# Performance work log

Hardware: AMD Instinct MI355X
Metric: run time of the kernel (lower is better)

The kernel has to match this reference:

```python
import jax, jax.numpy as jnp
import numpy as np

ROWS = 256
COLS = 256
EPS = 1e-8


def _radius_bins(rows, cols):
    # Same construction as SpectralLoss.__init__: integer radius per rfft bin,
    # ifftshifted along the row axis to match torch.rfft layout.
    shift_rows = rows // 2
    cols_onesided = cols // 2 + 1
    idx = np.indices((rows, cols_onesided)) - np.array([[[shift_rows]], [[0]]])
    r = np.sqrt(idx[0] ** 2 + idx[1] ** 2).astype(int)
    r = np.fft.ifftshift(r, axes=0)
    return r  # [rows, cols_onesided], values in [0, r_max]


def setup_inputs() -> dict:
    key = jax.random.key(0)
    k1, k2 = jax.random.split(key)
    r = _radius_bins(ROWS, COLS)
    vector_length = int(r.max()) + 1  # 182
    data = jax.random.normal(k1, (128, 3, ROWS, COLS), dtype=jnp.float32)
    mean = jax.random.uniform(k2, (vector_length,), dtype=jnp.float32)
    radius = jnp.asarray(r, dtype=jnp.int32)
    return {"data": data, "mean": mean, "radius": radius}


def reference(data, mean, radius):
    L = mean.shape[0]  # vector_length = r_max + 1
    # RGB -> luma (as in SpectralLoss.fft)
    gray = 0.299 * data[:, 0] + 0.587 * data[:, 1] + 0.114 * data[:, 2]  # [B,H,W]
    f = jnp.fft.rfft2(gray)  # [B, H, W//2+1]
    power = f.real ** 2 + f.imag ** 2  # sum of squared re/im parts
    fft_abs = 20.0 * jnp.log(power + EPS)  # [B, H, Wc]
    # Radial histogram: segment-mean keyed on integer radius (replaces the
    # original dense one-hot mask broadcast of shape [B, L, H, Wc]).
    seg = radius.reshape(-1)  # [N] with N = H*Wc
    B = fft_abs.shape[0]
    flat = fft_abs.reshape(B, -1).T  # [N, B]
    sums = jax.ops.segment_sum(flat, seg, num_segments=L)  # [L, B]
    counts = jax.ops.segment_sum(jnp.ones_like(flat[:, :1]), seg, num_segments=L)  # [L, 1]
    profile = (sums / counts).T  # [B, L]
    # Per-sample min-max normalization (same order of ops as torch code)
    profile = profile - jnp.min(profile, axis=1, keepdims=True)
    profile = profile / jnp.max(profile, axis=1, keepdims=True)
    # L1 loss with reduction='sum' against the target mean profile
    return jnp.sum(jnp.abs(profile - mean[None, :]))
```

## Files before the change

### kernel.cpp

```cpp
#include <hip/hip_runtime.h>
#include <cmath>

#define B_   128
#define H_   256
#define W_   256
#define WC_  129
#define L_   182
#define NG_  17
#define PI_F 3.14159265358979f

__device__ __forceinline__ void fft256x2_wave(float vr[8], float vi[8], int l) {
  float c0, s0;
  __sincosf(-2.f * PI_F * (float)l / 256.f, &s0, &c0);
  float c1 = s0, s1 = -c0;
  float c2 = c0 * c0 - s0 * s0, s2 = 2.f * c0 * s0;
  #pragma unroll
  for (int f = 0; f < 8; f += 4) {
    float ur = vr[f+0] + vr[f+2], ui = vi[f+0] + vi[f+2];
    float dr = vr[f+0] - vr[f+2], di = vi[f+0] - vi[f+2];
    vr[f+0] = ur; vi[f+0] = ui;
    vr[f+2] = dr * c0 - di * s0; vi[f+2] = dr * s0 + di * c0;
    ur = vr[f+1] + vr[f+3]; ui = vi[f+1] + vi[f+3];
    dr = vr[f+1] - vr[f+3]; di = vi[f+1] - vi[f+3];
    vr[f+1] = ur; vi[f+1] = ui;
    vr[f+3] = dr * c1 - di * s1; vi[f+3] = dr * s1 + di * c1;
    ur = vr[f+0] + vr[f+1]; ui = vi[f+0] + vi[f+1];
    dr = vr[f+0] - vr[f+1]; di = vi[f+0] - vi[f+1];
    vr[f+0] = ur; vi[f+0] = ui;
    vr[f+1] = dr * c2 - di * s2; vi[f+1] = dr * s2 + di * c2;
    ur = vr[f+2] + vr[f+3]; ui = vi[f+2] + vi[f+3];
    dr = vr[f+2] - vr[f+3]; di = vi[f+2] - vi[f+3];
    vr[f+2] = ur; vi[f+2] = ui;
    vr[f+3] = dr * c2 - di * s2; vi[f+3] = dr * s2 + di * c2;
  }
  #pragma unroll
  for (int h = 32; h >= 1; h >>= 1) {
    int i = l & (h - 1);
    float c, s;
    __sincosf(-PI_F * (float)i / (float)h, &s, &c);
    bool up = (l & h) != 0;
    float cc = up ? c : 1.f;
    float ss = up ? s : 0.f;
    float sgn = up ? -1.f : 1.f;
    #pragma unroll
    for (int j = 0; j < 8; ++j) {
      float br = __shfl_xor(vr[j], h, 64);
      float bi = __shfl_xor(vi[j], h, 64);
      float tr = fmaf(sgn, vr[j], br);
      float ti = fmaf(sgn, vi[j], bi);
      vr[j] = tr * cc - ti * ss;
      vi[j] = tr * ss + ti * cc;
    }
  }
}

#define P1_PAIRS 8
#define P1_STRIDE 259

__global__ __launch_bounds__(256) void pass1_kernel(
    const float* __restrict__ data, float4* __restrict__ inter4) {
  __shared__ float2 tile[P1_PAIRS * P1_STRIDE];
  int tid = threadIdx.x;
  int w = tid >> 6, l = tid & 63;
  int b = blockIdx.x >> 4;
  int row0 = (blockIdx.x & 15) * 16;
  const float* base = data + (size_t)b * 3 * (H_ * W_);
  float vr[8], vi[8];
  #pragma unroll
  for (int f = 0; f < 2; ++f) {
    int rowA = row0 + 2 * w + 8 * f;
    const float* pR = base + (size_t)rowA * W_;
    #pragma unroll
    for (int j = 0; j < 4; ++j) {
      int i = l + 64 * j;
      float r = pR[i], g = pR[H_ * W_ + i], bl = pR[2 * H_ * W_ + i];
      vr[4 * f + j] = fmaf(0.299f, r, fmaf(0.587f, g, 0.114f * bl));
      r = pR[W_ + i]; g = pR[H_ * W_ + W_ + i]; bl = pR[2 * H_ * W_ + W_ + i];
      vi[4 * f + j] = fmaf(0.299f, r, fmaf(0.587f, g, 0.114f * bl));
    }
  }
  fft256x2_wave(vr, vi, l);
  #pragma unroll
  for (int j = 0; j < 4; ++j) {
    tile[w * P1_STRIDE + l + 64 * j]       = make_float2(vr[j],     vi[j]);
    tile[(w + 4) * P1_STRIDE + l + 64 * j] = make_float2(vr[4 + j], vi[4 + j]);
  }
  __syncthreads();
  for (int f = tid; f < WC_ * P1_PAIRS; f += 256) {
    int k = f >> 3;
    int p = f & 7;
    int qk  = (int)(__brev((unsigned)k) >> 24);
    int qnk = (int)(__brev((unsigned)((256 - k) & 255)) >> 24);
    float2 Zk  = tile[p * P1_STRIDE + qk];
    float2 Znk = tile[p * P1_STRIDE + qnk];
    float4 o;
    o.x = 0.5f * (Zk.x + Znk.x);
    o.y = 0.5f * (Zk.y - Znk.y);
    o.z = 0.5f * (Zk.y + Znk.y);
    o.w = 0.5f * (Znk.x - Zk.x);
    inter4[((((size_t)b * WC_ + k) * H_ + row0) >> 1) + p] = o;
  }
}

__global__ __launch_bounds__(256) void pass2_kernel(
    const float2* __restrict__ inter, const int* __restrict__ radius,
    float* __restrict__ partial, float* __restrict__ cntpart) {
  __shared__ float lbins[L_];
  __shared__ float lcnt[L_];
  int tid = threadIdx.x;
  int wv = tid >> 6, l = tid & 63;
  int b = blockIdx.x / NG_;
  int g = blockIdx.x - b * NG_;
  int k1 = g * 8 + wv;
  int k2 = k1 + 4;
  bool v1 = k1 < WC_, v2 = k2 < WC_;
  bool do_cnt = (b == 0);
  for (int i = tid; i < L_; i += 256) lbins[i] = 0.f;
  if (do_cnt)
    for (int i = tid; i < L_; i += 256) lcnt[i] = 0.f;
  __syncthreads();
  float vr[8], vi[8];
  const float2* p1 = inter + ((size_t)b * WC_ + k1) * H_;
  const float2* p2 = inter + ((size_t)b * WC_ + k2) * H_;
  #pragma unroll
  for (int j = 0; j < 4; ++j) {
    float2 a = v1 ? p1[l + 64 * j] : make_float2(0.f, 0.f);
    float2 c = v2 ? p2[l + 64 * j] : make_float2(0.f, 0.f);
    vr[j] = a.x; vi[j] = a.y;
    vr[4 + j] = c.x; vi[4 + j] = c.y;
  }
  fft256x2_wave(vr, vi, l);
  int rb = 4 * (int)(__brev((unsigned)l) >> 26);
  #pragma unroll
  for (int j = 0; j < 4; ++j) {
    int rf = rb + ((j == 1) ? 2 : (j == 2) ? 1 : j);
    if (v1) {
      int bin = radius[rf * WC_ + k1];
      float pw = vr[j] * vr[j] + vi[j] * vi[j];
      atomicAdd(&lbins[bin], 20.f * __logf(pw + 1e-8f));
      if (do_cnt) atomicAdd(&lcnt[bin], 1.f);
    }
    if (v2) {
      int bin = radius[rf * WC_ + k2];
      float pw = vr[4 + j] * vr[4 + j] + vi[4 + j] * vi[4 + j];
      atomicAdd(&lbins[bin], 20.f * __logf(pw + 1e-8f));
      if (do_cnt) atomicAdd(&lcnt[bin], 1.f);
    }
  }
  __syncthreads();
  float* pp = partial + ((size_t)b * NG_ + g) * L_;
  for (int i = tid; i < L_; i += 256) pp[i] = lbins[i];
  if (do_cnt) {
    float* cp = cntpart + (size_t)g * L_;
    for (int i = tid; i < L_; i += 256) cp[i] = lcnt[i];
  }
}

__global__ __launch_bounds__(64) void loss_kernel(
    const float* __restrict__ partial, const float* __restrict__ cntpart,
    const float* __restrict__ mean, float* __restrict__ lpart) {
  int b = blockIdx.x;
  int l = threadIdx.x;
  const float* pb = partial + (size_t)b * NG_ * L_;
  float s0 = 0.f, s1 = 0.f, s2 = 0.f;
  float n0 = 0.f, n1 = 0.f, n2 = 0.f;
  #pragma unroll 1
  for (int g = 0; g < NG_; ++g) {
    s0 += pb[g * L_ + l];        n0 += cntpart[g * L_ + l];
    s1 += pb[g * L_ + l + 64];   n1 += cntpart[g * L_ + l + 64];
  }
  bool has2 = (l + 128) < L_;
  if (has2) {
    #pragma unroll 1
    for (int g = 0; g < NG_; ++g) {
      s2 += pb[g * L_ + l + 128];
      n2 += cntpart[g * L_ + l + 128];
    }
  }
  float pa = s0 / n0;
  float pc = s1 / n1;
  float pe = has2 ? (s2 / n2) : 0.f;
  float mn = fminf(pa, pc);
  if (has2) mn = fminf(mn, pe);
  #pragma unroll
  for (int h = 32; h >= 1; h >>= 1) mn = fminf(mn, __shfl_xor(mn, h, 64));
  float mxr = fmaxf(pa, pc);
  if (has2) mxr = fmaxf(mxr, pe);
  #pragma unroll
  for (int h = 32; h >= 1; h >>= 1) mxr = fmaxf(mxr, __shfl_xor(mxr, h, 64));
  float mx = mxr - mn;
  float s = fabsf((pa - mn) / mx - mean[l]) +
            fabsf((pc - mn) / mx - mean[l + 64]);
  if (has2) s += fabsf((pe - mn) / mx - mean[l + 128]);
  #pragma unroll
  for (int h = 32; h >= 1; h >>= 1) s += __shfl_xor(s, h, 64);
  if (l == 0) lpart[b] = s;
}

__global__ __launch_bounds__(64) void final_kernel(
    const float* __restrict__ lpart, float* __restrict__ out) {
  int l = threadIdx.x;
  float v = lpart[l] + lpart[l + 64];
  #pragma unroll
  for (int h = 32; h >= 1; h >>= 1) v += __shfl_xor(v, h, 64);
  if (l == 0) out[0] = v;
}

extern "C" void kernel_launch(void* const* d_in, const int* in_sizes, int n_in,
                              void* d_out, int out_size, void* d_ws, size_t ws_size,
                              hipStream_t stream) {
  const float* data   = (const float*)d_in[0];
  const float* mean   = (const float*)d_in[1];
  const int*   radius = (const int*)d_in[2];
  float* out = (float*)d_out;

  float2* inter = (float2*)d_ws;
  size_t inter_bytes = (size_t)B_ * WC_ * H_ * sizeof(float2);
  float* partial = (float*)((char*)d_ws + inter_bytes);
  float* cntpart = partial + (size_t)B_ * NG_ * L_;
  float* lpart   = cntpart + (size_t)NG_ * L_;

  pass1_kernel<<<B_ * 16, 256, 0, stream>>>(data, (float4*)inter);
  pass2_kernel<<<B_ * NG_, 256, 0, stream>>>(inter, radius, partial, cntpart);
  loss_kernel<<<B_, 64, 0, stream>>>(partial, cntpart, mean, lpart);
  final_kernel<<<1, 64, 0, stream>>>(lpart, out);
}
```

Before: 202.4 us.

## Vectorize luma loads through shared memory and fold final reduction into loss kernel

Pass1 now loads the 16-row RGB slab with coalesced float4 reads, computes luma into shared memory, then gathers FFT inputs from LDS instead of scalar strided global reads. The final single-block reduction kernel is removed; the last loss block, detected via an atomic counter reset in pass2, sums the per-sample losses. This cuts one kernel launch and improves global load width at the cost of extra LDS traffic and two barriers.

```diff
diff --git a/kernel.cpp b/kernel.cpp
--- a/kernel.cpp
+++ b/kernel.cpp
@@ -60,25 +60,38 @@
 __global__ __launch_bounds__(256) void pass1_kernel(
     const float* __restrict__ data, float4* __restrict__ inter4) {
   __shared__ float2 tile[P1_PAIRS * P1_STRIDE];
+  float* luma = (float*)tile;
   int tid = threadIdx.x;
   int w = tid >> 6, l = tid & 63;
   int b = blockIdx.x >> 4;
   int row0 = (blockIdx.x & 15) * 16;
-  const float* base = data + (size_t)b * 3 * (H_ * W_);
+  const float* base = data + (size_t)b * 3 * (H_ * W_) + (size_t)row0 * W_;
+  const float4* pr = (const float4*)base;
+  const float4* pg = (const float4*)(base + H_ * W_);
+  const float4* pb = (const float4*)(base + 2 * H_ * W_);
+  #pragma unroll
+  for (int it = 0; it < 4; ++it) {
+    int q = tid + 256 * it;
+    float4 r = pr[q], g = pg[q], bl = pb[q];
+    float4 o;
+    o.x = fmaf(0.299f, r.x, fmaf(0.587f, g.x, 0.114f * bl.x));
+    o.y = fmaf(0.299f, r.y, fmaf(0.587f, g.y, 0.114f * bl.y));
+    o.z = fmaf(0.299f, r.z, fmaf(0.587f, g.z, 0.114f * bl.z));
+    o.w = fmaf(0.299f, r.w, fmaf(0.587f, g.w, 0.114f * bl.w));
+    ((float4*)luma)[q] = o;
+  }
+  __syncthreads();
   float vr[8], vi[8];
   #pragma unroll
   for (int f = 0; f < 2; ++f) {
-    int rowA = row0 + 2 * w + 8 * f;
-    const float* pR = base + (size_t)rowA * W_;
+    int rA = 2 * w + 8 * f;
     #pragma unroll
     for (int j = 0; j < 4; ++j) {
-      int i = l + 64 * j;
-      float r = pR[i], g = pR[H_ * W_ + i], bl = pR[2 * H_ * W_ + i];
-      vr[4 * f + j] = fmaf(0.299f, r, fmaf(0.587f, g, 0.114f * bl));
-      r = pR[W_ + i]; g = pR[H_ * W_ + W_ + i]; bl = pR[2 * H_ * W_ + W_ + i];
-      vi[4 * f + j] = fmaf(0.299f, r, fmaf(0.587f, g, 0.114f * bl));
-    }
-  }
+      vr[4 * f + j] = luma[rA * W_ + l + 64 * j];
+      vi[4 * f + j] = luma[(rA + 1) * W_ + l + 64 * j];
+    }
+  }
+  __syncthreads();
   fft256x2_wave(vr, vi, l);
   #pragma unroll
   for (int j = 0; j < 4; ++j) {
@@ -104,13 +117,15 @@
 
 __global__ __launch_bounds__(256) void pass2_kernel(
     const float2* __restrict__ inter, const int* __restrict__ radius,
-    float* __restrict__ partial, float* __restrict__ cntpart) {
+    float* __restrict__ partial, float* __restrict__ cntpart,
+    unsigned* __restrict__ cnt_sync) {
   __shared__ float lbins[L_];
   __shared__ float lcnt[L_];
   int tid = threadIdx.x;
   int wv = tid >> 6, l = tid & 63;
   int b = blockIdx.x / NG_;
   int g = blockIdx.x - b * NG_;
+  if (blockIdx.x == 0 && tid == 0) cnt_sync[0] = 0u;
   int k1 = g * 8 + wv;
   int k2 = k1 + 4;
   bool v1 = k1 < WC_, v2 = k2 < WC_;
@@ -158,7 +173,8 @@
 
 __global__ __launch_bounds__(64) void loss_kernel(
     const float* __restrict__ partial, const float* __restrict__ cntpart,
-    const float* __restrict__ mean, float* __restrict__ lpart) {
+    const float* __restrict__ mean, float* __restrict__ lpart,
+    unsigned* __restrict__ cnt_sync, float* __restrict__ out) {
   int b = blockIdx.x;
   int l = threadIdx.x;
   const float* pb = partial + (size_t)b * NG_ * L_;
@@ -194,16 +210,24 @@
   if (has2) s += fabsf((pe - mn) / mx - mean[l + 128]);
   #pragma unroll
   for (int h = 32; h >= 1; h >>= 1) s += __shfl_xor(s, h, 64);
-  if (l == 0) lpart[b] = s;
-}
-
-__global__ __launch_bounds__(64) void final_kernel(
-    const float* __restrict__ lpart, float* __restrict__ out) {
-  int l = threadIdx.x;
-  float v = lpart[l] + lpart[l + 64];
-  #pragma unroll
-  for (int h = 32; h >= 1; h >>= 1) v += __shfl_xor(v, h, 64);
-  if (l == 0) out[0] = v;
+  int last = 0;
+  if (l == 0) {
+    lpart[b] = s;
+    __threadfence();
+    unsigned old = __hip_atomic_fetch_add(cnt_sync, 1u, __ATOMIC_ACQ_REL,
+                                          __HIP_MEMORY_SCOPE_AGENT);
+    last = (old == (unsigned)(B_ - 1));
+  }
+  last = __shfl(last, 0, 64);
+  if (last) {
+    float v = __hip_atomic_load(&lpart[l], __ATOMIC_ACQUIRE,
+                                __HIP_MEMORY_SCOPE_AGENT) +
+              __hip_atomic_load(&lpart[l + 64], __ATOMIC_ACQUIRE,
+                                __HIP_MEMORY_SCOPE_AGENT);
+    #pragma unroll
+    for (int h = 32; h >= 1; h >>= 1) v += __shfl_xor(v, h, 64);
+    if (l == 0) out[0] = v;
+  }
 }
 
 extern "C" void kernel_launch(void* const* d_in, const int* in_sizes, int n_in,
@@ -219,9 +243,10 @@
   float* partial = (float*)((char*)d_ws + inter_bytes);
   float* cntpart = partial + (size_t)B_ * NG_ * L_;
   float* lpart   = cntpart + (size_t)NG_ * L_;
+  unsigned* cnt_sync = (unsigned*)(lpart + B_);
 
   pass1_kernel<<<B_ * 16, 256, 0, stream>>>(data, (float4*)inter);
-  pass2_kernel<<<B_ * NG_, 256, 0, stream>>>(inter, radius, partial, cntpart);
-  loss_kernel<<<B_, 64, 0, stream>>>(partial, cntpart, mean, lpart);
-  final_kernel<<<1, 64, 0, stream>>>(lpart, out);
-}
+  pass2_kernel<<<B_ * NG_, 256, 0, stream>>>(inter, radius, partial, cntpart,
+                                             cnt_sync);
+  loss_kernel<<<B_, 64, 0, stream>>>(partial, cntpart, mean, lpart, cnt_sync, out);
+}
```

New measurement: 205.1 us. Within noise of the previous version (+1.3%).

## Fuse row and column FFT passes into one kernel with LDS spectrum

Applied to the files above, without the earlier changes.

Replaces the two-pass FFT (row FFT writing an intermediate spectrum to global memory, then column FFT) with a single kernel. Each 1024-thread block handles one image and a quarter of the column frequencies, recomputing the full row FFT and keeping its slice of the spectrum in shared memory. The real-to-complex split is now done with cross-lane shuffles instead of an LDS tile. This removes the global round trip of the intermediate spectrum, but every image's row FFTs and input reads are now repeated four times and LDS use per block is large, which limits occupancy.

```diff
diff --git a/kernel.cpp b/kernel.cpp
--- a/kernel.cpp
+++ b/kernel.cpp
@@ -6,7 +6,8 @@
 #define W_   256
 #define WC_  129
 #define L_   182
-#define NG_  17
+#define NGRP 4
+#define SPAD 258
 #define PI_F 3.14159265358979f
 
 __device__ __forceinline__ void fft256x2_wave(float vr[8], float vi[8], int l) {
@@ -54,106 +55,108 @@
   }
 }
 
-#define P1_PAIRS 8
-#define P1_STRIDE 259
-
-__global__ __launch_bounds__(256) void pass1_kernel(
-    const float* __restrict__ data, float4* __restrict__ inter4) {
-  __shared__ float2 tile[P1_PAIRS * P1_STRIDE];
-  int tid = threadIdx.x;
-  int w = tid >> 6, l = tid & 63;
-  int b = blockIdx.x >> 4;
-  int row0 = (blockIdx.x & 15) * 16;
-  const float* base = data + (size_t)b * 3 * (H_ * W_);
-  float vr[8], vi[8];
-  #pragma unroll
-  for (int f = 0; f < 2; ++f) {
-    int rowA = row0 + 2 * w + 8 * f;
-    const float* pR = base + (size_t)rowA * W_;
-    #pragma unroll
-    for (int j = 0; j < 4; ++j) {
-      int i = l + 64 * j;
-      float r = pR[i], g = pR[H_ * W_ + i], bl = pR[2 * H_ * W_ + i];
-      vr[4 * f + j] = fmaf(0.299f, r, fmaf(0.587f, g, 0.114f * bl));
-      r = pR[W_ + i]; g = pR[H_ * W_ + W_ + i]; bl = pR[2 * H_ * W_ + W_ + i];
-      vi[4 * f + j] = fmaf(0.299f, r, fmaf(0.587f, g, 0.114f * bl));
-    }
-  }
-  fft256x2_wave(vr, vi, l);
-  #pragma unroll
-  for (int j = 0; j < 4; ++j) {
-    tile[w * P1_STRIDE + l + 64 * j]       = make_float2(vr[j],     vi[j]);
-    tile[(w + 4) * P1_STRIDE + l + 64 * j] = make_float2(vr[4 + j], vi[4 + j]);
-  }
-  __syncthreads();
-  for (int f = tid; f < WC_ * P1_PAIRS; f += 256) {
-    int k = f >> 3;
-    int p = f & 7;
-    int qk  = (int)(__brev((unsigned)k) >> 24);
-    int qnk = (int)(__brev((unsigned)((256 - k) & 255)) >> 24);
-    float2 Zk  = tile[p * P1_STRIDE + qk];
-    float2 Znk = tile[p * P1_STRIDE + qnk];
-    float4 o;
-    o.x = 0.5f * (Zk.x + Znk.x);
-    o.y = 0.5f * (Zk.y - Znk.y);
-    o.z = 0.5f * (Zk.y + Znk.y);
-    o.w = 0.5f * (Znk.x - Zk.x);
-    inter4[((((size_t)b * WC_ + k) * H_ + row0) >> 1) + p] = o;
-  }
-}
-
-__global__ __launch_bounds__(256) void pass2_kernel(
-    const float2* __restrict__ inter, const int* __restrict__ radius,
+__global__ __launch_bounds__(1024, 8) void mega_kernel(
+    const float* __restrict__ data, const int* __restrict__ radius,
     float* __restrict__ partial, float* __restrict__ cntpart) {
+  __shared__ float specR[33 * SPAD];
+  __shared__ float specI[33 * SPAD];
   __shared__ float lbins[L_];
   __shared__ float lcnt[L_];
   int tid = threadIdx.x;
-  int wv = tid >> 6, l = tid & 63;
-  int b = blockIdx.x / NG_;
-  int g = blockIdx.x - b * NG_;
-  int k1 = g * 8 + wv;
-  int k2 = k1 + 4;
-  bool v1 = k1 < WC_, v2 = k2 < WC_;
+  int w = tid >> 6, l = tid & 63;
+  int rr = blockIdx.x >> 3;
+  int b = (blockIdx.x & 7) + 8 * (rr >> 2);
+  int c = rr & 3;
+  int s0 = c ? (32 * c + 1) : 0;
+  int ns = c ? 32 : 33;
   bool do_cnt = (b == 0);
-  for (int i = tid; i < L_; i += 256) lbins[i] = 0.f;
+  for (int i = tid; i < L_; i += 1024) { lbins[i] = 0.f; lcnt[i] = 0.f; }
+  const float* base = data + (size_t)b * 3 * (H_ * W_);
+  int p0 = l ? (3 * (1 << (31 - __clz(l))) - 1 - l) : 0;
+
+  for (int t = 0; t < 4; ++t) {
+    int pA = t * 32 + w;
+    int pB = pA + 16;
+    float vr[8], vi[8];
+    #pragma unroll
+    for (int j = 0; j < 4; ++j) {
+      int xx = l + 64 * j;
+      const float* q0 = base + (size_t)(2 * pA) * W_ + xx;
+      vr[j]     = fmaf(0.299f, q0[0],  fmaf(0.587f, q0[H_*W_],     0.114f * q0[2*H_*W_]));
+      vi[j]     = fmaf(0.299f, q0[W_], fmaf(0.587f, q0[H_*W_+W_],  0.114f * q0[2*H_*W_+W_]));
+      const float* q1 = base + (size_t)(2 * pB) * W_ + xx;
+      vr[4 + j] = fmaf(0.299f, q1[0],  fmaf(0.587f, q1[H_*W_],     0.114f * q1[2*H_*W_]));
+      vi[4 + j] = fmaf(0.299f, q1[W_], fmaf(0.587f, q1[H_*W_+W_],  0.114f * q1[2*H_*W_+W_]));
+    }
+    fft256x2_wave(vr, vi, l);
+    #pragma unroll
+    for (int f = 0; f < 8; f += 4) {
+      int pp = (f == 0) ? pA : pB;
+      float znr[4], zni[4];
+      znr[0] = __shfl(vr[f + 0], p0, 64);     zni[0] = __shfl(vi[f + 0], p0, 64);
+      znr[1] = __shfl_xor(vr[f + 1], 63, 64); zni[1] = __shfl_xor(vi[f + 1], 63, 64);
+      znr[2] = __shfl_xor(vr[f + 3], 63, 64); zni[2] = __shfl_xor(vi[f + 3], 63, 64);
+      znr[3] = __shfl_xor(vr[f + 2], 63, 64); zni[3] = __shfl_xor(vi[f + 2], 63, 64);
+      #pragma unroll
+      for (int j = 0; j < 4; ++j) {
+        int q = l + 64 * j;
+        int s = (q & 1) ? ((q == 1) ? 128 : -1) : (q >> 1);
+        int sl = s - s0;
+        if (s >= 0 && sl >= 0 && sl < ns) {
+          float2 R, I;
+          R.x = 0.5f * (vr[f + j] + znr[j]);
+          I.x = 0.5f * (vi[f + j] - zni[j]);
+          R.y = 0.5f * (vi[f + j] + zni[j]);
+          I.y = 0.5f * (znr[j] - vr[f + j]);
+          *(float2*)&specR[sl * SPAD + 2 * pp] = R;
+          *(float2*)&specI[sl * SPAD + 2 * pp] = I;
+        }
+      }
+    }
+  }
+  __syncthreads();
+
+  for (int t = 0; t < 2; ++t) {
+    if (t * 32 >= ns) break;
+    int sA = t * 32 + w, sB = sA + 16;
+    bool vA = sA < ns, vB = sB < ns;
+    int eA = vA ? sA : 0, eB = vB ? sB : 0;
+    float vr[8], vi[8];
+    #pragma unroll
+    for (int j = 0; j < 4; ++j) {
+      int y = l + 64 * j;
+      vr[j]     = specR[eA * SPAD + y];
+      vi[j]     = specI[eA * SPAD + y];
+      vr[4 + j] = specR[eB * SPAD + y];
+      vi[4 + j] = specI[eB * SPAD + y];
+    }
+    fft256x2_wave(vr, vi, l);
+    int sgA = s0 + eA, sgB = s0 + eB;
+    int kxA = (sgA == 128) ? 128 : (int)(__brev((unsigned)(2 * sgA)) >> 24);
+    int kxB = (sgB == 128) ? 128 : (int)(__brev((unsigned)(2 * sgB)) >> 24);
+    int rb = 4 * (int)(__brev((unsigned)l) >> 26);
+    #pragma unroll
+    for (int j = 0; j < 4; ++j) {
+      int ky = rb + ((j == 1) ? 2 : (j == 2) ? 1 : j);
+      if (vA) {
+        int bin = radius[ky * WC_ + kxA];
+        float pw = vr[j] * vr[j] + vi[j] * vi[j];
+        atomicAdd(&lbins[bin], 20.f * __logf(pw + 1e-8f));
+        if (do_cnt) atomicAdd(&lcnt[bin], 1.f);
+      }
+      if (vB) {
+        int bin = radius[ky * WC_ + kxB];
+        float pw = vr[4 + j] * vr[4 + j] + vi[4 + j] * vi[4 + j];
+        atomicAdd(&lbins[bin], 20.f * __logf(pw + 1e-8f));
+        if (do_cnt) atomicAdd(&lcnt[bin], 1.f);
+      }
+    }
+  }
+  __syncthreads();
+  float* pp = partial + ((size_t)b * NGRP + c) * L_;
+  for (int i = tid; i < L_; i += 1024) pp[i] = lbins[i];
   if (do_cnt)
-    for (int i = tid; i < L_; i += 256) lcnt[i] = 0.f;
-  __syncthreads();
-  float vr[8], vi[8];
-  const float2* p1 = inter + ((size_t)b * WC_ + k1) * H_;
-  const float2* p2 = inter + ((size_t)b * WC_ + k2) * H_;
-  #pragma unroll
-  for (int j = 0; j < 4; ++j) {
-    float2 a = v1 ? p1[l + 64 * j] : make_float2(0.f, 0.f);
-    float2 c = v2 ? p2[l + 64 * j] : make_float2(0.f, 0.f);
-    vr[j] = a.x; vi[j] = a.y;
-    vr[4 + j] = c.x; vi[4 + j] = c.y;
-  }
-  fft256x2_wave(vr, vi, l);
-  int rb = 4 * (int)(__brev((unsigned)l) >> 26);
-  #pragma unroll
-  for (int j = 0; j < 4; ++j) {
-    int rf = rb + ((j == 1) ? 2 : (j == 2) ? 1 : j);
-    if (v1) {
-      int bin = radius[rf * WC_ + k1];
-      float pw = vr[j] * vr[j] + vi[j] * vi[j];
-      atomicAdd(&lbins[bin], 20.f * __logf(pw + 1e-8f));
-      if (do_cnt) atomicAdd(&lcnt[bin], 1.f);
-    }
-    if (v2) {
-      int bin = radius[rf * WC_ + k2];
-      float pw = vr[4 + j] * vr[4 + j] + vi[4 + j] * vi[4 + j];
-      atomicAdd(&lbins[bin], 20.f * __logf(pw + 1e-8f));
-      if (do_cnt) atomicAdd(&lcnt[bin], 1.f);
-    }
-  }
-  __syncthreads();
-  float* pp = partial + ((size_t)b * NG_ + g) * L_;
-  for (int i = tid; i < L_; i += 256) pp[i] = lbins[i];
-  if (do_cnt) {
-    float* cp = cntpart + (size_t)g * L_;
-    for (int i = tid; i < L_; i += 256) cp[i] = lcnt[i];
-  }
+    for (int i = tid; i < L_; i += 1024) cntpart[c * L_ + i] = lcnt[i];
 }
 
 __global__ __launch_bounds__(64) void loss_kernel(
@@ -161,21 +164,15 @@
     const float* __restrict__ mean, float* __restrict__ lpart) {
   int b = blockIdx.x;
   int l = threadIdx.x;
-  const float* pb = partial + (size_t)b * NG_ * L_;
+  const float* pb = partial + (size_t)b * NGRP * L_;
   float s0 = 0.f, s1 = 0.f, s2 = 0.f;
   float n0 = 0.f, n1 = 0.f, n2 = 0.f;
-  #pragma unroll 1
-  for (int g = 0; g < NG_; ++g) {
+  bool has2 = (l + 128) < L_;
+  #pragma unroll
+  for (int g = 0; g < NGRP; ++g) {
     s0 += pb[g * L_ + l];        n0 += cntpart[g * L_ + l];
     s1 += pb[g * L_ + l + 64];   n1 += cntpart[g * L_ + l + 64];
-  }
-  bool has2 = (l + 128) < L_;
-  if (has2) {
-    #pragma unroll 1
-    for (int g = 0; g < NG_; ++g) {
-      s2 += pb[g * L_ + l + 128];
-      n2 += cntpart[g * L_ + l + 128];
-    }
+    if (has2) { s2 += pb[g * L_ + l + 128]; n2 += cntpart[g * L_ + l + 128]; }
   }
   float pa = s0 / n0;
   float pc = s1 / n1;
@@ -214,14 +211,11 @@
   const int*   radius = (const int*)d_in[2];
   float* out = (float*)d_out;
 
-  float2* inter = (float2*)d_ws;
-  size_t inter_bytes = (size_t)B_ * WC_ * H_ * sizeof(float2);
-  float* partial = (float*)((char*)d_ws + inter_bytes);
-  float* cntpart = partial + (size_t)B_ * NG_ * L_;
-  float* lpart   = cntpart + (size_t)NG_ * L_;
-
-  pass1_kernel<<<B_ * 16, 256, 0, stream>>>(data, (float4*)inter);
-  pass2_kernel<<<B_ * NG_, 256, 0, stream>>>(inter, radius, partial, cntpart);
+  float* partial = (float*)d_ws;
+  float* cntpart = partial + (size_t)B_ * NGRP * L_;
+  float* lpart   = cntpart + (size_t)NGRP * L_;
+
+  mega_kernel<<<B_ * NGRP, 1024, 0, stream>>>(data, radius, partial, cntpart);
   loss_kernel<<<B_, 64, 0, stream>>>(partial, cntpart, mean, lpart);
   final_kernel<<<1, 64, 0, stream>>>(lpart, out);
 }
```

Result: slower. 301.9 us (+49.1%).
